# Performance work log

Hardware: AMD Instinct MI355X
Metric: run time of the kernel (lower is better)

Reference implementation:

```python
import jax, jax.numpy as jnp
import numpy as np

NUM_HEADS = 12
HEAD_DIM = 64
LMBDA = 0.01
BLIND_SPOT = True


def setup_inputs() -> dict:
    key = jax.random.key(0)
    ks = jax.random.split(key, 4)
    B, S, D = 8, 1024, 768
    scale = 1.0 / np.sqrt(D)
    return {
        "hidden_states": jax.random.normal(ks[0], (B, S, D), jnp.float32),
        "attention_mask": jnp.zeros((B, 1, 1, S), jnp.float32),
        "Wq": jax.random.normal(ks[1], (D, D), jnp.float32) * scale,
        "bq": jnp.zeros((D,), jnp.float32),
        "Wk": jax.random.normal(ks[2], (D, D), jnp.float32) * scale,
        "bk": jnp.zeros((D,), jnp.float32),
        "Wv": jax.random.normal(ks[3], (D, D), jnp.float32) * scale,
        "bv": jnp.zeros((D,), jnp.float32),
    }


def _split_heads(x):
    B, S, D = x.shape
    return x.reshape(B, S, NUM_HEADS, HEAD_DIM).transpose(0, 2, 1, 3)  # [B,H,S,dh]


def reference(hidden_states, attention_mask, Wq, bq, Wk, bk, Wv, bv):
    B, S, D = hidden_states.shape
    q = _split_heads(hidden_states @ Wq + bq)
    k = _split_heads(hidden_states @ Wk + bk)
    v = _split_heads(hidden_states @ Wv + bv)

    scores = jnp.einsum("bhqd,bhkd->bhqk", q, k)  # [B,H,S,S]
    if BLIND_SPOT:
        # zero out the diagonal BEFORE scaling (matches original order)
        eye = jnp.eye(S, dtype=scores.dtype)
        scores = scores * (1.0 - eye)
    scores = scores / np.sqrt(HEAD_Dim() if False else HEAD_DIM).astype(np.float32)
    scores = scores + attention_mask  # additive mask, broadcast [B,1,1,S]

    # auxiliary diagonal-weighted regularization loss
    if LMBDA != 0.0:
        diag_vals = jnp.diagonal(scores, axis1=-2, axis2=-1)  # [B,H,S]
        loss = LMBDA * jnp.sum(diag_vals)
    else:
        loss = jnp.float32(0.0)

    probs = jax.nn.softmax(scores, axis=-1)  # dropout = identity (eval)
    context = jnp.einsum("bhqk,bhkd->bhqd", probs, v)  # [B,H,S,dh]
    context = context.transpose(0, 2, 1, 3).reshape(B, S, D)
    return context, loss
```

## Files before the change

kernel.cpp:

```cpp
#include <hip/hip_runtime.h>
#include <hip/hip_bf16.h>
#include <stdint.h>

#define Bb 8
#define Ss 1024
#define Dd 768
#define Hh 12
#define DH 64

typedef __attribute__((ext_vector_type(8))) short bf16x8;
typedef __attribute__((ext_vector_type(4))) float f32x4;

static __device__ __forceinline__ unsigned short f2b(float x) {
    union { float f; unsigned u; } v; v.f = x;
    unsigned r = v.u + 0x7FFFu + ((v.u >> 16) & 1u);
    return (unsigned short)(r >> 16);
}

static __device__ __forceinline__ void gll16(const void* g, void* l) {
    __builtin_amdgcn_global_load_lds((const __attribute__((address_space(1))) void*)g,
                                     (__attribute__((address_space(3))) void*)l,
                                     16, 0, 0);
}

__global__ __launch_bounds__(256) void k_prep(
    const float* __restrict__ hs,
    const float* __restrict__ Wq, const float* __restrict__ Wk, const float* __restrict__ Wv,
    const float* __restrict__ mask,
    unsigned short* __restrict__ hb, unsigned short* __restrict__ Wt,
    float* __restrict__ loss_out) {
    __shared__ float tile[32][33];
    __shared__ float red[4];
    const int bid = blockIdx.x;
    const int tid = threadIdx.x;
    if (bid < 6144) {
        const int i = (bid * 256 + tid) * 4;
        const float4 v = *reinterpret_cast<const float4*>(hs + i);
        ushort4 o;
        o.x = f2b(v.x); o.y = f2b(v.y); o.z = f2b(v.z); o.w = f2b(v.w);
        *reinterpret_cast<ushort4*>(hb + i) = o;
    } else if (bid < 7872) {
        const int t = bid - 6144;
        const int w = t / 576, rem = t % 576;
        const int k0 = (rem / 24) * 32, n0 = (rem % 24) * 32;
        const float* W = (w == 0) ? Wq : (w == 1) ? Wk : Wv;
        const int c = tid & 31, r0 = tid >> 5;
        #pragma unroll
        for (int i = 0; i < 4; ++i)
            tile[r0 + i * 8][c] = W[(size_t)(k0 + r0 + i * 8) * Dd + n0 + c];
        __syncthreads();
        unsigned short* o = Wt + (size_t)w * Dd * Dd;
        #pragma unroll
        for (int i = 0; i < 4; ++i)
            o[(size_t)(n0 + r0 + i * 8) * Dd + k0 + c] = f2b(tile[c][r0 + i * 8]);
    } else {
        float s = 0.f;
        for (int i = tid; i < Bb * Ss; i += 256) s += mask[i];
        #pragma unroll
        for (int d = 1; d < 64; d <<= 1) s += __shfl_xor(s, d);
        const int lane = tid & 63, wv = tid >> 6;
        if (lane == 0) red[wv] = s;
        __syncthreads();
        if (tid == 0)
            loss_out[0] = 0.01f * 12.f * (red[0] + red[1] + red[2] + red[3]);
    }
}

__global__ __launch_bounds__(256) void k_qkv(
    const unsigned short* __restrict__ hb,
    const unsigned short* __restrict__ Wt,
    const float* __restrict__ bq, const float* __restrict__ bk, const float* __restrict__ bv,
    unsigned short* __restrict__ Qo, unsigned short* __restrict__ Ko,
    unsigned short* __restrict__ Vo) {
    __shared__ __align__(16) unsigned short Al[2][4096];
    __shared__ __align__(16) unsigned short Bl[2][4096];
    const int bid = blockIdx.x;
    const int x = bid & 7, local = bid >> 3;
    const int mt = x * 8 + (local & 7);
    const int nt = local >> 3;
    const int m0 = mt * 128, n0 = nt * 128;
    const int w  = nt / 6;
    const int tid = threadIdx.x, lane = tid & 63, wv = tid >> 6;
    const int l15 = lane & 15, l4 = lane >> 4;
    const int wm = (wv >> 1) * 64, wn = (wv & 1) * 64;

    f32x4 acc[4][4];
    #pragma unroll
    for (int i = 0; i < 4; ++i)
        #pragma unroll
        for (int j = 0; j < 4; ++j)
            acc[i][j] = f32x4{0.f, 0.f, 0.f, 0.f};

    const int ldr = lane >> 2;
    const int ldc = (lane & 3) * 8;

    #define STAGE(buf, kt)                                                              \
        {                                                                               \
            const int k0_ = (kt) * 32;                                                  \
            _Pragma("unroll")                                                           \
            for (int i_ = 0; i_ < 2; ++i_) {                                            \
                const int c_ = wv * 2 + i_;                                             \
                gll16(hb + (size_t)(m0 + c_ * 16 + ldr) * Dd + k0_ + ldc, &Al[buf][c_ * 512]); \
                gll16(Wt + (size_t)(n0 + c_ * 16 + ldr) * Dd + k0_ + ldc, &Bl[buf][c_ * 512]); \
            }                                                                           \
        }

    #define COMPUTE(buf)                                                                \
        {                                                                               \
            bf16x8 af_[4], bf_[4];                                                      \
            _Pragma("unroll")                                                           \
            for (int i_ = 0; i_ < 4; ++i_) {                                            \
                af_[i_] = *reinterpret_cast<const bf16x8*>(&Al[buf][(wm + i_ * 16 + l15) * 32 + l4 * 8]); \
                bf_[i_] = *reinterpret_cast<const bf16x8*>(&Bl[buf][(wn + i_ * 16 + l15) * 32 + l4 * 8]); \
            }                                                                           \
            _Pragma("unroll")                                                           \
            for (int i_ = 0; i_ < 4; ++i_)                                              \
                _Pragma("unroll")                                                       \
                for (int j_ = 0; j_ < 4; ++j_)                                          \
                    acc[i_][j_] = __builtin_amdgcn_mfma_f32_16x16x32_bf16(af_[i_], bf_[j_], acc[i_][j_], 0, 0, 0); \
        }

    STAGE(0, 0);
    __syncthreads();
    int buf = 0;
    for (int kt = 1; kt < Dd / 32; ++kt) {
        STAGE(buf ^ 1, kt);
        COMPUTE(buf);
        __syncthreads();
        buf ^= 1;
    }
    COMPUTE(buf);
    #undef STAGE
    #undef COMPUTE

    const float* bias = (w == 0) ? bq : (w == 1) ? bk : bv;
    if (w < 2) {
        unsigned short* O = (w == 0) ? Qo : Ko;
        #pragma unroll
        for (int j = 0; j < 4; ++j) {
            const int nL = n0 + wn + j * 16 + l15 - w * Dd;
            const float bs = bias[nL];
            const int hh = nL >> 6, d = nL & 63;
            #pragma unroll
            for (int i = 0; i < 4; ++i) {
                const int mb = m0 + wm + i * 16 + l4 * 4;
                #pragma unroll
                for (int r = 0; r < 4; ++r) {
                    const int m = mb + r;
                    const int b = m >> 10, s = m & 1023;
                    O[(((size_t)b * Hh + hh) * Ss + s) * DH + d] = f2b(acc[i][j][r] + bs);
                }
            }
        }
    } else {
        #pragma unroll
        for (int j = 0; j < 4; ++j) {
            const int nL = n0 + wn + j * 16 + l15 - 2 * Dd;
            const float bs = bias[nL];
            const int hh = nL >> 6, d = nL & 63;
            #pragma unroll
            for (int i = 0; i < 4; ++i) {
                const int m = m0 + wm + i * 16 + l4 * 4;
                const int b = m >> 10, s = m & 1023;
                ushort4 o;
                o.x = f2b(acc[i][j][0] + bs);
                o.y = f2b(acc[i][j][1] + bs);
                o.z = f2b(acc[i][j][2] + bs);
                o.w = f2b(acc[i][j][3] + bs);
                *reinterpret_cast<ushort4*>(Vo + (((size_t)b * Hh + hh) * DH + d) * Ss + s) = o;
            }
        }
    }
}

__global__ __launch_bounds__(256) void k_attn(
    const unsigned short* __restrict__ Q,
    const unsigned short* __restrict__ K,
    const unsigned short* __restrict__ VT,
    const float* __restrict__ mask,
    float* __restrict__ out) {
    __shared__ __align__(16) unsigned short Kl[64 * 64];
    __shared__ __align__(16) unsigned short Vl[64 * 64];
    __shared__ __align__(16) unsigned short Pl[4][16][72];
    __shared__ __align__(16) float Ml[1024];

    const int bid = blockIdx.x;
    const int wg  = (bid & 7) * 192 + (bid >> 3);
    const int bh  = wg >> 4;
    const int qt  = wg & 15;
    const int b = bh / Hh, h = bh % Hh;
    const int tid = threadIdx.x, lane = tid & 63, wv = tid >> 6;
    const int l15 = lane & 15, l4 = lane >> 4;
    const int q0 = qt * 64 + wv * 16;

    const unsigned short* Qb = Q + (size_t)bh * Ss * DH;
    const unsigned short* Kb = K + (size_t)bh * Ss * DH;
    const unsigned short* Vb = VT + (size_t)bh * DH * Ss;
    const float* mb = mask + (size_t)b * Ss;

    {
        const float4 mv = *reinterpret_cast<const float4*>(mb + tid * 4);
        float4 ms;
        ms.x = mv.x * 1.44269504f; ms.y = mv.y * 1.44269504f;
        ms.z = mv.z * 1.44269504f; ms.w = mv.w * 1.44269504f;
        *reinterpret_cast<float4*>(&Ml[tid * 4]) = ms;
    }

    const bf16x8 qf0 = *reinterpret_cast<const bf16x8*>(Qb + (q0 + l15) * DH + l4 * 8);
    const bf16x8 qf1 = *reinterpret_cast<const bf16x8*>(Qb + (q0 + l15) * DH + 32 + l4 * 8);

    float m2 = -3.0e38f, lsum = 0.f;
    f32x4 oacc[4];
    #pragma unroll
    for (int dt = 0; dt < 4; ++dt) oacc[dt] = f32x4{0.f, 0.f, 0.f, 0.f};

    const float C1 = 0.125f * 1.44269504f;

    const int srow = lane >> 3;
    const int sslt = lane & 7;

    for (int kt = 0; kt < Ss / 64; ++kt) {
        {
            const int r0 = wv * 16;
            #pragma unroll
            for (int i = 0; i < 2; ++i) {
                const int rK = r0 + i * 8 + srow;
                const int gsK = sslt ^ (rK & 7);
                gll16(Kb + (size_t)(kt * 64 + rK) * DH + gsK * 8, Kl + (r0 + i * 8) * 64);
                gll16(Vb + (size_t)rK * Ss + kt * 64 + gsK * 8,   Vl + (r0 + i * 8) * 64);
            }
        }
        __syncthreads();

        f32x4 sc[4];
        #pragma unroll
        for (int ct = 0; ct < 4; ++ct) {
            const int kr = ct * 16 + l15;
            const int sw = kr & 7;
            const bf16x8 kf0 = *reinterpret_cast<const bf16x8*>(Kl + kr * 64 + ((l4 ^ sw) * 8));
            const bf16x8 kf1 = *reinterpret_cast<const bf16x8*>(Kl + kr * 64 + (((l4 + 4) ^ sw) * 8));
            f32x4 a = f32x4{0.f, 0.f, 0.f, 0.f};
            a = __builtin_amdgcn_mfma_f32_16x16x32_bf16(kf0, qf0, a, 0, 0, 0);
            a = __builtin_amdgcn_mfma_f32_16x16x32_bf16(kf1, qf1, a, 0, 0, 0);
            sc[ct] = a;
        }

        float4 mk[4];
        #pragma unroll
        for (int ct = 0; ct < 4; ++ct)
            mk[ct] = *reinterpret_cast<const float4*>(&Ml[kt * 64 + ct * 16 + l4 * 4]);

        float p[16];
        float pmax = -3.0e38f;
        const bool dk = (kt == qt);
        #pragma unroll
        for (int ct = 0; ct < 4; ++ct) {
            const float* mkp = reinterpret_cast<const float*>(&mk[ct]);
            #pragma unroll
            for (int r = 0; r < 4; ++r) {
                float t = fmaf(sc[ct][r], C1, mkp[r]);
                if (dk && (ct * 16 + l4 * 4 + r) == (wv * 16 + l15)) t = mkp[r];
                p[ct * 4 + r] = t;
                pmax = fmaxf(pmax, t);
            }
        }
        pmax = fmaxf(pmax, __shfl_xor(pmax, 16));
        pmax = fmaxf(pmax, __shfl_xor(pmax, 32));

        if (__any(pmax > m2 + 10.f)) {
            const float mnew = fmaxf(m2, pmax);
            const float alpha = __builtin_amdgcn_exp2f(m2 - mnew);
            m2 = mnew;
            lsum *= alpha;
            float ar[4];
            #pragma unroll
            for (int r = 0; r < 4; ++r) ar[r] = __shfl(alpha, l4 * 4 + r);
            #pragma unroll
            for (int dt = 0; dt < 4; ++dt)
                #pragma unroll
                for (int r = 0; r < 4; ++r) oacc[dt][r] *= ar[r];
        }

        float rs = 0.f;
        #pragma unroll
        for (int i = 0; i < 16; ++i) {
            const float e = __builtin_amdgcn_exp2f(p[i] - m2);
            p[i] = e;
            rs += e;
        }
        rs += __shfl_xor(rs, 16);
        rs += __shfl_xor(rs, 32);
        lsum += rs;

        #pragma unroll
        for (int ct = 0; ct < 4; ++ct) {
            unsigned lo, hi;
            asm("v_cvt_pk_bf16_f32 %0, %1, %2" : "=v"(lo) : "v"(p[ct * 4 + 0]), "v"(p[ct * 4 + 1]));
            asm("v_cvt_pk_bf16_f32 %0, %1, %2" : "=v"(hi) : "v"(p[ct * 4 + 2]), "v"(p[ct * 4 + 3]));
            *reinterpret_cast<uint2*>(&Pl[wv][l15][ct * 16 + l4 * 4]) = make_uint2(lo, hi);
        }

        const bf16x8 pf0 = *reinterpret_cast<const bf16x8*>(&Pl[wv][l15][l4 * 8]);
        const bf16x8 pf1 = *reinterpret_cast<const bf16x8*>(&Pl[wv][l15][32 + l4 * 8]);
        #pragma unroll
        for (int dt = 0; dt < 4; ++dt) {
            const int vr = dt * 16 + l15;
            const int sv = vr & 7;
            const bf16x8 vf0 = *reinterpret_cast<const bf16x8*>(Vl + vr * 64 + ((l4 ^ sv) * 8));
            const bf16x8 vf1 = *reinterpret_cast<const bf16x8*>(Vl + vr * 64 + (((l4 + 4) ^ sv) * 8));
            oacc[dt] = __builtin_amdgcn_mfma_f32_16x16x32_bf16(pf0, vf0, oacc[dt], 0, 0, 0);
            oacc[dt] = __builtin_amdgcn_mfma_f32_16x16x32_bf16(pf1, vf1, oacc[dt], 0, 0, 0);
        }
        __syncthreads();
    }

    #pragma unroll
    for (int r = 0; r < 4; ++r) {
        const float li = __shfl(lsum, l4 * 4 + r);
        const float inv = 1.f / li;
        const int s = qt * 64 + wv * 16 + l4 * 4 + r;
        float* op = out + ((size_t)b * Ss + s) * Dd + h * DH;
        #pragma unroll
        for (int dt = 0; dt < 4; ++dt)
            op[dt * 16 + l15] = oacc[dt][r] * inv;
    }
}

extern "C" void kernel_launch(void* const* d_in, const int* in_sizes, int n_in,
                              void* d_out, int out_size, void* d_ws, size_t ws_size,
                              hipStream_t stream) {
    const float* hs   = (const float*)d_in[0];
    const float* mask = (const float*)d_in[1];
    const float* Wq   = (const float*)d_in[2];
    const float* bq   = (const float*)d_in[3];
    const float* Wk   = (const float*)d_in[4];
    const float* bk   = (const float*)d_in[5];
    const float* Wv   = (const float*)d_in[6];
    const float* bv   = (const float*)d_in[7];
    float* out = (float*)d_out;

    uint8_t* ws = (uint8_t*)d_ws;
    unsigned short* hb = (unsigned short*)(ws);
    unsigned short* Wt = (unsigned short*)(ws + 12582912);
    unsigned short* Qw = (unsigned short*)(ws + 16121856);
    unsigned short* Kw = (unsigned short*)(ws + 28704768);
    unsigned short* Vw = (unsigned short*)(ws + 41287680);

    hipLaunchKernelGGL(k_prep, dim3(7873), dim3(256), 0, stream,
                       hs, Wq, Wk, Wv, mask, hb, Wt, out + 6291456);
    hipLaunchKernelGGL(k_qkv,  dim3(1152), dim3(256), 0, stream,
                       hb, Wt, bq, bk, bv, Qw, Kw, Vw);
    hipLaunchKernelGGL(k_attn, dim3(1536), dim3(256), 0, stream, Qw, Kw, Vw, mask, out);
}
```

Before: 215.2 us.

## Double-buffer K/V tiles in attention and reorder QKV GEMM LDS layout

The attention kernel now double-buffers the K and V tiles in LDS and prefetches tile kt+1 while computing tile kt, replacing the load-then-sync pattern at the top of each iteration. The QKV GEMM changes its LDS staging layout so each wave's fragment read is a contiguous 16-byte chunk per lane, which is meant to avoid LDS bank conflicts. This doubles K/V LDS usage, which may lower occupancy. The attention loop also relies on the existing end-of-iteration barrier to order the prefetched writes before they are read.

```diff
diff --git a/kernel.cpp b/kernel.cpp
--- a/kernel.cpp
+++ b/kernel.cpp
@@ -83,6 +83,7 @@
     const int tid = threadIdx.x, lane = tid & 63, wv = tid >> 6;
     const int l15 = lane & 15, l4 = lane >> 4;
     const int wm = (wv >> 1) * 64, wn = (wv & 1) * 64;
+    const int wmw = (wv >> 1) * 4, wnw = (wv & 1) * 4;
 
     f32x4 acc[4][4];
     #pragma unroll
@@ -91,8 +92,8 @@
         for (int j = 0; j < 4; ++j)
             acc[i][j] = f32x4{0.f, 0.f, 0.f, 0.f};
 
-    const int ldr = lane >> 2;
-    const int ldc = (lane & 3) * 8;
+    const int srow = lane & 15;
+    const int sk   = lane >> 4;
 
     #define STAGE(buf, kt)                                                              \
         {                                                                               \
@@ -100,8 +101,8 @@
             _Pragma("unroll")                                                           \
             for (int i_ = 0; i_ < 2; ++i_) {                                            \
                 const int c_ = wv * 2 + i_;                                             \
-                gll16(hb + (size_t)(m0 + c_ * 16 + ldr) * Dd + k0_ + ldc, &Al[buf][c_ * 512]); \
-                gll16(Wt + (size_t)(n0 + c_ * 16 + ldr) * Dd + k0_ + ldc, &Bl[buf][c_ * 512]); \
+                gll16(hb + (size_t)(m0 + c_ * 16 + srow) * Dd + k0_ + sk * 8, &Al[buf][c_ * 512]); \
+                gll16(Wt + (size_t)(n0 + c_ * 16 + srow) * Dd + k0_ + sk * 8, &Bl[buf][c_ * 512]); \
             }                                                                           \
         }
 
@@ -110,8 +111,8 @@
             bf16x8 af_[4], bf_[4];                                                      \
             _Pragma("unroll")                                                           \
             for (int i_ = 0; i_ < 4; ++i_) {                                            \
-                af_[i_] = *reinterpret_cast<const bf16x8*>(&Al[buf][(wm + i_ * 16 + l15) * 32 + l4 * 8]); \
-                bf_[i_] = *reinterpret_cast<const bf16x8*>(&Bl[buf][(wn + i_ * 16 + l15) * 32 + l4 * 8]); \
+                af_[i_] = *reinterpret_cast<const bf16x8*>(&Al[buf][(wmw + i_) * 512 + (l4 * 16 + l15) * 8]); \
+                bf_[i_] = *reinterpret_cast<const bf16x8*>(&Bl[buf][(wnw + i_) * 512 + (l4 * 16 + l15) * 8]); \
             }                                                                           \
             _Pragma("unroll")                                                           \
             for (int i_ = 0; i_ < 4; ++i_)                                              \
@@ -179,8 +180,8 @@
     const unsigned short* __restrict__ VT,
     const float* __restrict__ mask,
     float* __restrict__ out) {
-    __shared__ __align__(16) unsigned short Kl[64 * 64];
-    __shared__ __align__(16) unsigned short Vl[64 * 64];
+    __shared__ __align__(16) unsigned short Kl[2][4096];
+    __shared__ __align__(16) unsigned short Vl[2][4096];
     __shared__ __align__(16) unsigned short Pl[4][16][72];
     __shared__ __align__(16) float Ml[1024];
 
@@ -198,6 +199,21 @@
     const unsigned short* Vb = VT + (size_t)bh * DH * Ss;
     const float* mb = mask + (size_t)b * Ss;
 
+    const int srow = lane >> 3;
+    const int sslt = lane & 7;
+
+    #define AST(buf, kt)                                                               \
+        {                                                                              \
+            const int r0_ = wv * 16;                                                   \
+            _Pragma("unroll")                                                          \
+            for (int i_ = 0; i_ < 2; ++i_) {                                           \
+                const int rK_ = r0_ + i_ * 8 + srow;                                   \
+                const int gs_ = sslt ^ (rK_ & 7);                                      \
+                gll16(Kb + (size_t)((kt) * 64 + rK_) * DH + gs_ * 8, &Kl[buf][(r0_ + i_ * 8) * 64]); \
+                gll16(Vb + (size_t)rK_ * Ss + (kt) * 64 + gs_ * 8,   &Vl[buf][(r0_ + i_ * 8) * 64]); \
+            }                                                                          \
+        }
+
     {
         const float4 mv = *reinterpret_cast<const float4*>(mb + tid * 4);
         float4 ms;
@@ -205,9 +221,11 @@
         ms.z = mv.z * 1.44269504f; ms.w = mv.w * 1.44269504f;
         *reinterpret_cast<float4*>(&Ml[tid * 4]) = ms;
     }
+    AST(0, 0);
 
     const bf16x8 qf0 = *reinterpret_cast<const bf16x8*>(Qb + (q0 + l15) * DH + l4 * 8);
     const bf16x8 qf1 = *reinterpret_cast<const bf16x8*>(Qb + (q0 + l15) * DH + 32 + l4 * 8);
+    __syncthreads();
 
     float m2 = -3.0e38f, lsum = 0.f;
     f32x4 oacc[4];
@@ -215,30 +233,18 @@
     for (int dt = 0; dt < 4; ++dt) oacc[dt] = f32x4{0.f, 0.f, 0.f, 0.f};
 
     const float C1 = 0.125f * 1.44269504f;
-
-    const int srow = lane >> 3;
-    const int sslt = lane & 7;
+    int buf = 0;
 
     for (int kt = 0; kt < Ss / 64; ++kt) {
-        {
-            const int r0 = wv * 16;
-            #pragma unroll
-            for (int i = 0; i < 2; ++i) {
-                const int rK = r0 + i * 8 + srow;
-                const int gsK = sslt ^ (rK & 7);
-                gll16(Kb + (size_t)(kt * 64 + rK) * DH + gsK * 8, Kl + (r0 + i * 8) * 64);
-                gll16(Vb + (size_t)rK * Ss + kt * 64 + gsK * 8,   Vl + (r0 + i * 8) * 64);
-            }
-        }
-        __syncthreads();
+        if (kt < Ss / 64 - 1) AST(buf ^ 1, kt + 1);
 
         f32x4 sc[4];
         #pragma unroll
         for (int ct = 0; ct < 4; ++ct) {
             const int kr = ct * 16 + l15;
             const int sw = kr & 7;
-            const bf16x8 kf0 = *reinterpret_cast<const bf16x8*>(Kl + kr * 64 + ((l4 ^ sw) * 8));
-            const bf16x8 kf1 = *reinterpret_cast<const bf16x8*>(Kl + kr * 64 + (((l4 + 4) ^ sw) * 8));
+            const bf16x8 kf0 = *reinterpret_cast<const bf16x8*>(&Kl[buf][kr * 64 + ((l4 ^ sw) * 8)]);
+            const bf16x8 kf1 = *reinterpret_cast<const bf16x8*>(&Kl[buf][kr * 64 + (((l4 + 4) ^ sw) * 8)]);
             f32x4 a = f32x4{0.f, 0.f, 0.f, 0.f};
             a = __builtin_amdgcn_mfma_f32_16x16x32_bf16(kf0, qf0, a, 0, 0, 0);
             a = __builtin_amdgcn_mfma_f32_16x16x32_bf16(kf1, qf1, a, 0, 0, 0);
@@ -306,13 +312,15 @@
         for (int dt = 0; dt < 4; ++dt) {
             const int vr = dt * 16 + l15;
             const int sv = vr & 7;
-            const bf16x8 vf0 = *reinterpret_cast<const bf16x8*>(Vl + vr * 64 + ((l4 ^ sv) * 8));
-            const bf16x8 vf1 = *reinterpret_cast<const bf16x8*>(Vl + vr * 64 + (((l4 + 4) ^ sv) * 8));
+            const bf16x8 vf0 = *reinterpret_cast<const bf16x8*>(&Vl[buf][vr * 64 + ((l4 ^ sv) * 8)]);
+            const bf16x8 vf1 = *reinterpret_cast<const bf16x8*>(&Vl[buf][vr * 64 + (((l4 + 4) ^ sv) * 8)]);
             oacc[dt] = __builtin_amdgcn_mfma_f32_16x16x32_bf16(pf0, vf0, oacc[dt], 0, 0, 0);
             oacc[dt] = __builtin_amdgcn_mfma_f32_16x16x32_bf16(pf1, vf1, oacc[dt], 0, 0, 0);
         }
         __syncthreads();
-    }
+        buf ^= 1;
+    }
+    #undef AST
 
     #pragma unroll
     for (int r = 0; r < 4; ++r) {
```

Result: slower. 234.1 us (+8.8%).
